# Performance work log

Measured on AMD Instinct MI355X. Metric: run time of the kernel, lower is better.

Reference implementation:

```python
import jax, jax.numpy as jnp
import numpy as np

N_NODES = 50000
N_EDGES = 800000
D_MODEL = 128
N_HEADS = 4
N_LAYERS = 2
F_HEAD = D_MODEL // N_HEADS


def setup_inputs() -> dict:
    key = jax.random.key(0)
    ks = jax.random.split(key, 6)
    x = jax.random.normal(ks[0], (N_NODES, D_MODEL), dtype=jnp.float32)
    edge_index = jax.random.randint(ks[1], (2, N_EDGES), 0, N_NODES, dtype=jnp.int64)
    scale = 1.0 / np.sqrt(D_MODEL)
    W = jax.random.normal(ks[2], (N_LAYERS, D_MODEL, D_MODEL), dtype=jnp.float32) * scale
    a_src = jax.random.normal(ks[3], (N_LAYERS, N_HEADS, F_HEAD), dtype=jnp.float32) * scale
    a_dst = jax.random.normal(ks[4], (N_LAYERS, N_HEADS, F_HEAD), dtype=jnp.float32) * scale
    b = jnp.zeros((N_LAYERS, D_MODEL), dtype=jnp.float32)
    return {"x": x, "edge_index": edge_index, "W": W, "a_src": a_src, "a_dst": a_dst, "b": b}


def _gat_layer(x, src, dst, W_l, a_src_l, a_dst_l, b_l, apply_act):
    N = x.shape[0]
    H, F = a_src_l.shape
    # projected node features, split into heads: [N, H, F]
    h = (x @ W_l).reshape(N, H, F)
    # per-node attention contributions: [N, H]
    alpha_s = jnp.einsum("nhf,hf->nh", h, a_src_l)
    alpha_d = jnp.einsum("nhf,hf->nh", h, a_dst_l)
    # per-edge raw scores, LeakyReLU(0.2): [E, H]
    e = jax.nn.leaky_relu(alpha_s[src] + alpha_d[dst], negative_slope=0.2)
    # numerically-stable segment softmax over edges grouped by target node
    e_max = jax.ops.segment_max(e, dst, num_segments=N)
    e_exp = jnp.exp(e - e_max[dst])
    denom = jax.ops.segment_sum(e_exp, dst, num_segments=N)
    alpha = e_exp / (denom[dst] + 1e-16)  # [E, H]
    # gather source features, weight, scatter-add to targets
    msg = h[src] * alpha[:, :, None]  # [E, H, F]
    out = jax.ops.segment_sum(msg, dst, num_segments=N).reshape(N, H * F)
    out = out + x + b_l  # skip connection (dims match) + bias
    return jax.nn.elu(out) if apply_act else out


def reference(x, edge_index, W, a_src, a_dst, b):
    src, dst = edge_index[0], edge_index[1]
    L = W.shape[0]
    for l in range(L):
        x = _gat_layer(x, src, dst, W[l], a_src[l], a_dst[l], b[l], apply_act=(l < L - 1))
    return x
```

## Files before the change

### kernel.cpp

```cpp
#include <hip/hip_runtime.h>
#include <math.h>

constexpr int NN = 50000;
constexpr int NE = 800000;
constexpr int D  = 128;
constexpr int NH = 4;
constexpr int NBUK = (NN + 255) / 256;
constexpr int CAP  = 4608;
constexpr int FR_PER_LAYER = 9 * 4 * 64;

typedef __attribute__((ext_vector_type(8))) short short8v;
typedef __attribute__((ext_vector_type(4))) float f32x4;

__device__ inline unsigned short rne_bf16(float f) {
    unsigned bits = __float_as_uint(f);
    return (unsigned short)((bits + 0x7FFFu + ((bits >> 16) & 1u)) >> 16);
}

#define DOT2BF(accv, pa, pb) \
    asm("v_dot2_f32_bf16 %0, %1, %2, %0" : "+v"(accv) : "v"(pa), "v"(pb))

__global__ __launch_bounds__(256) void partition_kernel(
    const int* __restrict__ src, const int* __restrict__ dst,
    int* __restrict__ bwp, unsigned* __restrict__ bukbuf)
{
    __shared__ int cnt[NBUK];
    __shared__ int run[NBUK];
    for (int i = threadIdx.x; i < NBUK; i += 256) cnt[i] = 0;
    __syncthreads();
    const int base = blockIdx.x * 2048;
    int s_[8], b_[8], dl_[8];
    #pragma unroll
    for (int i = 0; i < 8; ++i) {
        int e = base + i * 256 + threadIdx.x;
        bool ok = (e < NE);
        s_[i] = ok ? src[e] : 0;
        int d = ok ? dst[e] : 0;
        b_[i] = d >> 8; dl_[i] = d & 255;
        if (ok) atomicAdd(&cnt[b_[i]], 1);
    }
    __syncthreads();
    for (int i = threadIdx.x; i < NBUK; i += 256)
        run[i] = cnt[i] ? atomicAdd(&bwp[i], cnt[i]) : 0;
    __syncthreads();
    #pragma unroll
    for (int i = 0; i < 8; ++i) {
        int e = base + i * 256 + threadIdx.x;
        if (e < NE) {
            int pos = atomicAdd(&run[b_[i]], 1);
            if (pos < CAP)
                bukbuf[b_[i] * CAP + pos] = (unsigned)s_[i] | ((unsigned)dl_[i] << 16);
        }
    }
}

__global__ __launch_bounds__(256) void bucket_sort_kernel(
    const unsigned* __restrict__ bukbuf, const int* __restrict__ bwp,
    int2* __restrict__ rowse, unsigned short* __restrict__ srcs)
{
    const int b = blockIdx.x;
    const int t = threadIdx.x;
    const int cnt = min(bwp[b], CAP);
    const int base = b * CAP;
    __shared__ int hist[256];
    __shared__ int run[256];
    __shared__ int s[256];
    __shared__ unsigned short stage[CAP];
    hist[t] = 0;
    __syncthreads();
    for (int i = t; i < cnt; i += 256)
        atomicAdd(&hist[bukbuf[base + i] >> 16], 1);
    __syncthreads();
    int v = hist[t];
    s[t] = v;
    __syncthreads();
    for (int off = 1; off < 256; off <<= 1) {
        int u = (t >= off) ? s[t - off] : 0;
        __syncthreads();
        s[t] += u;
        __syncthreads();
    }
    const int excl = s[t] - v;
    const int node = b * 256 + t;
    if (node < NN) {
        int2 se; se.x = base + excl; se.y = base + excl + v;
        rowse[node] = se;
    }
    run[t] = excl;
    __syncthreads();
    for (int i = t; i < cnt; i += 256) {
        unsigned p = bukbuf[base + i];
        int pos = atomicAdd(&run[p >> 16], 1);
        stage[pos] = (unsigned short)(p & 0xFFFFu);
    }
    __syncthreads();
    for (int i = t; i < cnt; i += 256) srcs[base + i] = stage[i];
}

__global__ __launch_bounds__(256) void repack_kernel(
    const float* __restrict__ W, const float* __restrict__ a_src,
    const float* __restrict__ a_dst, unsigned short* __restrict__ Wpk,
    int* __restrict__ bwp)
{
    if (blockIdx.x == 0 && threadIdx.x < NBUK) bwp[threadIdx.x] = 0;
    int tid = blockIdx.x * 256 + threadIdx.x;
    if (tid >= 2 * FR_PER_LAYER) return;
    int layer = tid / FR_PER_LAYER;
    int rest  = tid % FR_PER_LAYER;
    int tile  = rest >> 8;
    int kstep = (rest >> 6) & 3;
    int lane  = rest & 63;
    int col   = lane & 15;
    int kbase = kstep * 32 + (lane >> 4) * 8;
    const float* Wl = W + (size_t)layer * D * D;
    unsigned short v[8];
    if (tile < 8) {
        int c = tile * 16 + col;
        #pragma unroll
        for (int j = 0; j < 8; ++j) v[j] = rne_bf16(Wl[(kbase + j) * D + c]);
    } else {
        #pragma unroll
        for (int j = 0; j < 8; ++j) v[j] = 0;
        if (col < 8) {
            const float* av = ((col < 4) ? a_src : a_dst) + layer * D + (col & 3) * 32;
            const int hbase = (col & 3) * 32;
            for (int j = 0; j < 8; ++j) {
                float sum = 0.f;
                const float* wr = Wl + (size_t)(kbase + j) * D + hbase;
                #pragma unroll
                for (int jj = 0; jj < 32; ++jj) sum = fmaf(wr[jj], av[jj], sum);
                v[j] = rne_bf16(sum);
            }
        }
    }
    *(uint4*)(Wpk + (size_t)tid * 8) = *(const uint4*)v;
}

template<int BF16IN>
__global__ __launch_bounds__(256) void gemm_alpha_kernel(
    const void* __restrict__ xin, const unsigned short* __restrict__ Wpk,
    unsigned short* __restrict__ hb, float* __restrict__ alpha_s,
    float* __restrict__ alpha_d)
{
    __shared__ unsigned short xl[64 * 128];
    const int t = threadIdx.x;
    const int row0 = blockIdx.x * 64;

    if constexpr (BF16IN) {
        const unsigned short* xb = (const unsigned short*)xin;
        #pragma unroll
        for (int it = 0; it < 4; ++it) {
            int idx = it * 256 + t;
            int r   = idx >> 4;
            int c8  = (idx & 15) * 8;
            int n   = row0 + r;
            uint4 v = {0u, 0u, 0u, 0u};
            if (n < NN) v = *(const uint4*)(xb + (size_t)n * D + c8);
            *(uint4*)(xl + r * 128 + (c8 ^ ((r & 7) << 3))) = v;
        }
    } else {
        const float* xf = (const float*)xin;
        #pragma unroll
        for (int it = 0; it < 8; ++it) {
            int idx = it * 256 + t;
            int r   = idx >> 5;
            int c4  = (idx & 31) * 4;
            int n   = row0 + r;
            float4 v;
            if (n < NN) v = *(const float4*)(xf + (size_t)n * D + c4);
            else { v.x = 0.f; v.y = 0.f; v.z = 0.f; v.w = 0.f; }
            unsigned p0 = ((unsigned)rne_bf16(v.y) << 16) | rne_bf16(v.x);
            unsigned p1 = ((unsigned)rne_bf16(v.w) << 16) | rne_bf16(v.z);
            uint2 pv; pv.x = p0; pv.y = p1;
            *(uint2*)(xl + r * 128 + (c4 ^ ((r & 7) << 3))) = pv;
        }
    }
    __syncthreads();

    const int wv  = t >> 6;
    const int l   = t & 63;
    const int l15 = l & 15;
    const int g   = l >> 4;
    const int strip = wv * 16;
    const int arow  = strip + l15;

    f32x4 acc[9];
    #pragma unroll
    for (int i = 0; i < 9; ++i) acc[i] = (f32x4){0.f, 0.f, 0.f, 0.f};

    #pragma unroll
    for (int ks = 0; ks < 4; ++ks) {
        const int k0 = ks * 32 + g * 8;
        short8v a = *(const short8v*)(xl + arow * 128 + (k0 ^ ((arow & 7) << 3)));
        #pragma unroll
        for (int tl = 0; tl < 9; ++tl) {
            short8v b = *(const short8v*)(Wpk + ((size_t)(tl * 4 + ks) * 64 + l) * 8);
            acc[tl] = __builtin_amdgcn_mfma_f32_16x16x32_bf16(a, b, acc[tl], 0, 0, 0);
        }
    }

    #pragma unroll
    for (int r = 0; r < 4; ++r) {
        const int n = row0 + strip + g * 4 + r;
        if (n < NN) {
            #pragma unroll
            for (int tl = 0; tl < 8; ++tl)
                hb[(size_t)n * D + tl * 16 + l15] = rne_bf16(acc[tl][r]);
            const float av = acc[8][r];
            if (l15 < 4)      alpha_s[n * NH + l15]       = av;
            else if (l15 < 8) alpha_d[n * NH + (l15 - 4)] = av;
        }
    }
}

#define SHUF2(MI, SA, SB, WP) {                                          \
    int eA = lb + (MI), eB = eA + 1;                                     \
    SA = __shfl(msrc, eA); SB = __shfl(msrc, eB);                        \
    unsigned a01 = (unsigned)__shfl((int)uw01, eA);                      \
    unsigned a23 = (unsigned)__shfl((int)uw23, eA);                      \
    unsigned c01 = (unsigned)__shfl((int)uw01, eB);                      \
    unsigned c23 = (unsigned)__shfl((int)uw23, eB);                      \
    unsigned uwA = (head < 2) ? a01 : a23;                               \
    unsigned uwB = (head < 2) ? c01 : c23;                               \
    WP = __builtin_amdgcn_perm(uwB, uwA, wsel); }

#define ROWLD(S) (*(const uint4*)(hb + ((size_t)(S) << 7) + (ql << 3)))

#define DOT2BLOCK(WP, HA, HB) {                                               \
    DOT2BF(den, WP, ones);                                                    \
    unsigned p_;                                                              \
    p_ = __builtin_amdgcn_perm(HB.x, HA.x, 0x05040100u); DOT2BF(acc[0], p_, WP); \
    p_ = __builtin_amdgcn_perm(HB.x, HA.x, 0x07060302u); DOT2BF(acc[1], p_, WP); \
    p_ = __builtin_amdgcn_perm(HB.y, HA.y, 0x05040100u); DOT2BF(acc[2], p_, WP); \
    p_ = __builtin_amdgcn_perm(HB.y, HA.y, 0x07060302u); DOT2BF(acc[3], p_, WP); \
    p_ = __builtin_amdgcn_perm(HB.z, HA.z, 0x05040100u); DOT2BF(acc[4], p_, WP); \
    p_ = __builtin_amdgcn_perm(HB.z, HA.z, 0x07060302u); DOT2BF(acc[5], p_, WP); \
    p_ = __builtin_amdgcn_perm(HB.w, HA.w, 0x05040100u); DOT2BF(acc[6], p_, WP); \
    p_ = __builtin_amdgcn_perm(HB.w, HA.w, 0x07060302u); DOT2BF(acc[7], p_, WP); }

template<int IN_BF16, int OUT_BF16, int ACT>
__global__ __launch_bounds__(256) void gather_kernel(
    const unsigned short* __restrict__ hb, const float* __restrict__ alpha_s,
    const float* __restrict__ alpha_d, const int2* __restrict__ rowse,
    const unsigned short* __restrict__ srcs, const void* __restrict__ x_in,
    const float* __restrict__ bias, void* __restrict__ out)
{
    const int lane = threadIdx.x & 63;
    const int q    = lane >> 4;
    const int ql   = lane & 15;
    const int head = ql >> 2;
    const int lb   = q * 16;
    const int n = blockIdx.x * 16 + (threadIdx.x >> 6) * 4 + q;
    if (n >= NN) return;

    const int2 se = rowse[n];
    const int start = se.x, end = se.y;
    const float4 ad4 = *(const float4*)&alpha_d[n * NH];
    const unsigned wsel = (head & 1) ? 0x07060302u : 0x05040100u;
    const unsigned ones = 0x3F803F80u;

    float acc[8];
    #pragma unroll
    for (int c = 0; c < 8; ++c) acc[c] = 0.f;
    float den = 0.f;

    for (int base = start; base < end; base += 16) {
        const int cnt = min(16, end - base);
        int msrc = 0;
        unsigned uw01 = 0, uw23 = 0;
        if (ql < cnt) {
            msrc = srcs[base + ql];
            const float4 as4 = *(const float4*)&alpha_s[msrc * NH];
            float e0 = as4.x + ad4.x; e0 = (e0 > 0.f) ? e0 : 0.2f * e0;
            float e1 = as4.y + ad4.y; e1 = (e1 > 0.f) ? e1 : 0.2f * e1;
            float e2 = as4.z + ad4.z; e2 = (e2 > 0.f) ? e2 : 0.2f * e2;
            float e3 = as4.w + ad4.w; e3 = (e3 > 0.f) ? e3 : 0.2f * e3;
            float w0 = __expf(e0), w1 = __expf(e1);
            float w2 = __expf(e2), w3 = __expf(e3);
            uw01 = ((unsigned)rne_bf16(w1) << 16) | rne_bf16(w0);
            uw23 = ((unsigned)rne_bf16(w3) << 16) | rne_bf16(w2);
        }
        const int mm = (cnt + 1) & ~1;

        int sxa, sxb, sya, syb;
        unsigned wpX, wpY;
        uint4 hxa, hxb, hya, hyb;
        SHUF2(0, sxa, sxb, wpX);
        hxa = ROWLD(sxa); hxb = ROWLD(sxb);
        if (mm > 2) {
            SHUF2(2, sya, syb, wpY);
            hya = ROWLD(sya); hyb = ROWLD(syb);
        }
        int m = 0;
        while (true) {
            DOT2BLOCK(wpX, hxa, hxb);
            m += 2;
            if (m >= mm) break;
            if (m + 2 < mm) {
                SHUF2(m + 2, sxa, sxb, wpX);
                hxa = ROWLD(sxa); hxb = ROWLD(sxb);
            }
            DOT2BLOCK(wpY, hya, hyb);
            m += 2;
            if (m >= mm) break;
            if (m + 2 < mm) {
                SHUF2(m + 2, sya, syb, wpY);
                hya = ROWLD(sya); hyb = ROWLD(syb);
            }
        }
    }

    const float inv = 1.f / (den + 1e-16f);
    const size_t o8 = (size_t)n * D + ql * 8;
    float xi[8];
    if constexpr (IN_BF16) {
        const uint4 xv = *(const uint4*)((const unsigned short*)x_in + o8);
        xi[0] = __uint_as_float(xv.x << 16);
        xi[1] = __uint_as_float(xv.x & 0xFFFF0000u);
        xi[2] = __uint_as_float(xv.y << 16);
        xi[3] = __uint_as_float(xv.y & 0xFFFF0000u);
        xi[4] = __uint_as_float(xv.z << 16);
        xi[5] = __uint_as_float(xv.z & 0xFFFF0000u);
        xi[6] = __uint_as_float(xv.w << 16);
        xi[7] = __uint_as_float(xv.w & 0xFFFF0000u);
    } else {
        const float4 a = *(const float4*)((const float*)x_in + o8);
        const float4 b = *(const float4*)((const float*)x_in + o8 + 4);
        xi[0]=a.x; xi[1]=a.y; xi[2]=a.z; xi[3]=a.w;
        xi[4]=b.x; xi[5]=b.y; xi[6]=b.z; xi[7]=b.w;
    }
    const float4 ba = *(const float4*)(bias + ql * 8);
    const float4 bb = *(const float4*)(bias + ql * 8 + 4);
    const float bi[8] = {ba.x, ba.y, ba.z, ba.w, bb.x, bb.y, bb.z, bb.w};
    float o[8];
    #pragma unroll
    for (int c = 0; c < 8; ++c) {
        float v = fmaf(acc[c], inv, xi[c]) + bi[c];
        if constexpr (ACT) v = (v > 0.f) ? v : (__expf(v) - 1.f);
        o[c] = v;
    }
    if constexpr (OUT_BF16) {
        unsigned short ov[8];
        #pragma unroll
        for (int c = 0; c < 8; ++c) ov[c] = rne_bf16(o[c]);
        *(uint4*)((unsigned short*)out + o8) = *(const uint4*)ov;
    } else {
        float4 oa = {o[0], o[1], o[2], o[3]};
        float4 ob = {o[4], o[5], o[6], o[7]};
        *(float4*)((float*)out + o8)     = oa;
        *(float4*)((float*)out + o8 + 4) = ob;
    }
}

extern "C" void kernel_launch(void* const* d_in, const int* in_sizes, int n_in,
                              void* d_out, int out_size, void* d_ws, size_t ws_size,
                              hipStream_t stream) {
    const float* x     = (const float*)d_in[0];
    const int*   ei    = (const int*)d_in[1];
    const float* W     = (const float*)d_in[2];
    const float* a_src = (const float*)d_in[3];
    const float* a_dst = (const float*)d_in[4];
    const float* bias  = (const float*)d_in[5];
    float* outp = (float*)d_out;

    const int* e_src = ei;
    const int* e_dst = ei + NE;

    char* base = (char*)d_ws;
    unsigned short* hb  = (unsigned short*)(base);
    unsigned short* x1b = (unsigned short*)(base + 12800000);
    float* al_s      = (float*)(base + 25600000);
    float* al_d      = (float*)(base + 26400000);
    int2*  rowse     = (int2*) (base + 27200000);
    unsigned short* srcs = (unsigned short*)(base + 27600000);
    unsigned* bukbuf = (unsigned*)(base + 29406336);
    int*   bwp       = (int*)  (base + 33019008);
    unsigned short* Wpk = (unsigned short*)(base + 33019792);

    const int rblocks = (2 * FR_PER_LAYER + 255) / 256;
    repack_kernel<<<rblocks, 256, 0, stream>>>(W, a_src, a_dst, Wpk, bwp);
    const int pblocks = (NE + 2047) / 2048;
    partition_kernel<<<pblocks, 256, 0, stream>>>(e_src, e_dst, bwp, bukbuf);
    bucket_sort_kernel<<<NBUK, 256, 0, stream>>>(bukbuf, bwp, rowse, srcs);

    const int gemm_blocks   = (NN + 63) / 64;
    const int gather_blocks = (NN + 15) / 16;

    gemm_alpha_kernel<0><<<gemm_blocks, 256, 0, stream>>>(x, Wpk, hb, al_s, al_d);
    gather_kernel<0, 1, 1><<<gather_blocks, 256, 0, stream>>>(
        hb, al_s, al_d, rowse, srcs, x, bias, x1b);
    gemm_alpha_kernel<1><<<gemm_blocks, 256, 0, stream>>>(
        x1b, Wpk + (size_t)FR_PER_LAYER * 8, hb, al_s, al_d);
    gather_kernel<1, 0, 0><<<gather_blocks, 256, 0, stream>>>(
        hb, al_s, al_d, rowse, srcs, x1b, bias + D, outp);
}
```

Before: 134.0 us.

## Fuse edge partition with weight repack and bucket sort with first GEMM

```diff
diff --git a/kernel.cpp b/kernel.cpp
--- a/kernel.cpp
+++ b/kernel.cpp
@@ -6,8 +6,11 @@
 constexpr int D  = 128;
 constexpr int NH = 4;
 constexpr int NBUK = (NN + 255) / 256;
-constexpr int CAP  = 4608;
+constexpr int EPB  = 2048;
+constexpr int NPB  = (NE + EPB - 1) / EPB;
+constexpr int CAPS = 4608;
 constexpr int FR_PER_LAYER = 9 * 4 * 64;
+constexpr int RBLK = (2 * FR_PER_LAYER) / 256;
 
 typedef __attribute__((ext_vector_type(8))) short short8v;
 typedef __attribute__((ext_vector_type(4))) float f32x4;
@@ -20,91 +23,10 @@
 #define DOT2BF(accv, pa, pb) \
     asm("v_dot2_f32_bf16 %0, %1, %2, %0" : "+v"(accv) : "v"(pa), "v"(pb))
 
-__global__ __launch_bounds__(256) void partition_kernel(
-    const int* __restrict__ src, const int* __restrict__ dst,
-    int* __restrict__ bwp, unsigned* __restrict__ bukbuf)
-{
-    __shared__ int cnt[NBUK];
-    __shared__ int run[NBUK];
-    for (int i = threadIdx.x; i < NBUK; i += 256) cnt[i] = 0;
-    __syncthreads();
-    const int base = blockIdx.x * 2048;
-    int s_[8], b_[8], dl_[8];
-    #pragma unroll
-    for (int i = 0; i < 8; ++i) {
-        int e = base + i * 256 + threadIdx.x;
-        bool ok = (e < NE);
-        s_[i] = ok ? src[e] : 0;
-        int d = ok ? dst[e] : 0;
-        b_[i] = d >> 8; dl_[i] = d & 255;
-        if (ok) atomicAdd(&cnt[b_[i]], 1);
-    }
-    __syncthreads();
-    for (int i = threadIdx.x; i < NBUK; i += 256)
-        run[i] = cnt[i] ? atomicAdd(&bwp[i], cnt[i]) : 0;
-    __syncthreads();
-    #pragma unroll
-    for (int i = 0; i < 8; ++i) {
-        int e = base + i * 256 + threadIdx.x;
-        if (e < NE) {
-            int pos = atomicAdd(&run[b_[i]], 1);
-            if (pos < CAP)
-                bukbuf[b_[i] * CAP + pos] = (unsigned)s_[i] | ((unsigned)dl_[i] << 16);
-        }
-    }
-}
-
-__global__ __launch_bounds__(256) void bucket_sort_kernel(
-    const unsigned* __restrict__ bukbuf, const int* __restrict__ bwp,
-    int2* __restrict__ rowse, unsigned short* __restrict__ srcs)
-{
-    const int b = blockIdx.x;
-    const int t = threadIdx.x;
-    const int cnt = min(bwp[b], CAP);
-    const int base = b * CAP;
-    __shared__ int hist[256];
-    __shared__ int run[256];
-    __shared__ int s[256];
-    __shared__ unsigned short stage[CAP];
-    hist[t] = 0;
-    __syncthreads();
-    for (int i = t; i < cnt; i += 256)
-        atomicAdd(&hist[bukbuf[base + i] >> 16], 1);
-    __syncthreads();
-    int v = hist[t];
-    s[t] = v;
-    __syncthreads();
-    for (int off = 1; off < 256; off <<= 1) {
-        int u = (t >= off) ? s[t - off] : 0;
-        __syncthreads();
-        s[t] += u;
-        __syncthreads();
-    }
-    const int excl = s[t] - v;
-    const int node = b * 256 + t;
-    if (node < NN) {
-        int2 se; se.x = base + excl; se.y = base + excl + v;
-        rowse[node] = se;
-    }
-    run[t] = excl;
-    __syncthreads();
-    for (int i = t; i < cnt; i += 256) {
-        unsigned p = bukbuf[base + i];
-        int pos = atomicAdd(&run[p >> 16], 1);
-        stage[pos] = (unsigned short)(p & 0xFFFFu);
-    }
-    __syncthreads();
-    for (int i = t; i < cnt; i += 256) srcs[base + i] = stage[i];
-}
-
-__global__ __launch_bounds__(256) void repack_kernel(
-    const float* __restrict__ W, const float* __restrict__ a_src,
-    const float* __restrict__ a_dst, unsigned short* __restrict__ Wpk,
-    int* __restrict__ bwp)
-{
-    if (blockIdx.x == 0 && threadIdx.x < NBUK) bwp[threadIdx.x] = 0;
-    int tid = blockIdx.x * 256 + threadIdx.x;
-    if (tid >= 2 * FR_PER_LAYER) return;
+__device__ __forceinline__ void repack_body(
+    int tid, const float* __restrict__ W, const float* __restrict__ a_src,
+    const float* __restrict__ a_dst, unsigned short* __restrict__ Wpk)
+{
     int layer = tid / FR_PER_LAYER;
     int rest  = tid % FR_PER_LAYER;
     int tile  = rest >> 8;
@@ -136,15 +58,75 @@
     *(uint4*)(Wpk + (size_t)tid * 8) = *(const uint4*)v;
 }
 
+__global__ __launch_bounds__(256) void prep_kernel(
+    const float* __restrict__ W, const float* __restrict__ a_src,
+    const float* __restrict__ a_dst, unsigned short* __restrict__ Wpk,
+    const int* __restrict__ src, const int* __restrict__ dst,
+    unsigned* __restrict__ outbuf, int* __restrict__ cnts,
+    int* __restrict__ lofs)
+{
+    __shared__ union {
+        struct { unsigned stage[EPB]; int cnt[NBUK]; int fill[NBUK]; int sc[256]; } p;
+        int dummy;
+    } sm;
+    if (blockIdx.x < RBLK) {
+        repack_body(blockIdx.x * 256 + threadIdx.x, W, a_src, a_dst, Wpk);
+        return;
+    }
+    const int pb = blockIdx.x - RBLK;
+    const int t  = threadIdx.x;
+    for (int i = t; i < NBUK; i += 256) sm.p.cnt[i] = 0;
+    __syncthreads();
+    const int base = pb * EPB;
+    const int tot  = min(NE - base, EPB);
+    unsigned pk[8]; int bk[8];
+    #pragma unroll
+    for (int i = 0; i < 8; ++i) {
+        int e = base + i * 256 + t;
+        bool ok = (e < NE);
+        int s = ok ? src[e] : 0;
+        int d = ok ? dst[e] : 0;
+        bk[i] = d >> 8;
+        pk[i] = (unsigned)s | ((unsigned)(d & 255) << 16) | ((unsigned)bk[i] << 24);
+        if (ok) atomicAdd(&sm.p.cnt[bk[i]], 1);
+    }
+    __syncthreads();
+    int v = (t < NBUK) ? sm.p.cnt[t] : 0;
+    sm.p.sc[t] = v;
+    __syncthreads();
+    for (int off = 1; off < 256; off <<= 1) {
+        int u = (t >= off) ? sm.p.sc[t - off] : 0;
+        __syncthreads();
+        sm.p.sc[t] += u;
+        __syncthreads();
+    }
+    const int excl = sm.p.sc[t] - v;
+    if (t < NBUK) {
+        sm.p.fill[t] = excl;
+        cnts[t * NPB + pb] = v;
+        lofs[t * NPB + pb] = excl;
+    }
+    __syncthreads();
+    #pragma unroll
+    for (int i = 0; i < 8; ++i) {
+        int e = base + i * 256 + t;
+        if (e < NE) {
+            int pos = atomicAdd(&sm.p.fill[bk[i]], 1);
+            sm.p.stage[pos] = pk[i];
+        }
+    }
+    __syncthreads();
+    for (int i = t; i < tot; i += 256) outbuf[base + i] = sm.p.stage[i];
+}
+
 template<int BF16IN>
-__global__ __launch_bounds__(256) void gemm_alpha_kernel(
-    const void* __restrict__ xin, const unsigned short* __restrict__ Wpk,
-    unsigned short* __restrict__ hb, float* __restrict__ alpha_s,
-    float* __restrict__ alpha_d)
-{
-    __shared__ unsigned short xl[64 * 128];
+__device__ __forceinline__ void gemm_body(
+    int blk, unsigned short* __restrict__ xl, const void* __restrict__ xin,
+    const unsigned short* __restrict__ Wpk, unsigned short* __restrict__ hb,
+    float* __restrict__ alpha_s, float* __restrict__ alpha_d)
+{
     const int t = threadIdx.x;
-    const int row0 = blockIdx.x * 64;
+    const int row0 = blk * 64;
 
     if constexpr (BF16IN) {
         const unsigned short* xb = (const unsigned short*)xin;
@@ -211,6 +193,77 @@
             else if (l15 < 8) alpha_d[n * NH + (l15 - 4)] = av;
         }
     }
+}
+
+template<int BF16IN>
+__global__ __launch_bounds__(256) void sort_gemm_kernel(
+    const unsigned* __restrict__ outbuf, const int* __restrict__ cnts,
+    const int* __restrict__ lofs, int2* __restrict__ rowse,
+    unsigned short* __restrict__ srcs, const void* __restrict__ xin,
+    const unsigned short* __restrict__ Wpk, unsigned short* __restrict__ hb,
+    float* __restrict__ alpha_s, float* __restrict__ alpha_d)
+{
+    __shared__ union {
+        struct { unsigned stage[CAPS]; int hist[256]; int run[256]; int sc[256]; int cursor; } s;
+        unsigned short xl[64 * 128];
+    } sm;
+
+    if (blockIdx.x >= NBUK) {
+        gemm_body<BF16IN>(blockIdx.x - NBUK, sm.xl, xin, Wpk, hb, alpha_s, alpha_d);
+        return;
+    }
+    const int b = blockIdx.x;
+    const int t = threadIdx.x;
+    if (t == 0) sm.s.cursor = 0;
+    sm.s.hist[t] = 0;
+    __syncthreads();
+    for (int pb = t; pb < NPB; pb += 256) {
+        int len = cnts[b * NPB + pb];
+        if (len > 0) {
+            int off = lofs[b * NPB + pb];
+            int pos = atomicAdd(&sm.s.cursor, len);
+            const unsigned* sp = outbuf + pb * EPB + off;
+            for (int k = 0; k < len; ++k)
+                if (pos + k < CAPS) sm.s.stage[pos + k] = sp[k];
+        }
+    }
+    __syncthreads();
+    const int tot = min(sm.s.cursor, CAPS);
+    for (int i = t; i < tot; i += 256)
+        atomicAdd(&sm.s.hist[(sm.s.stage[i] >> 16) & 255], 1);
+    __syncthreads();
+    int v = sm.s.hist[t];
+    sm.s.sc[t] = v;
+    __syncthreads();
+    for (int off = 1; off < 256; off <<= 1) {
+        int u = (t >= off) ? sm.s.sc[t - off] : 0;
+        __syncthreads();
+        sm.s.sc[t] += u;
+        __syncthreads();
+    }
+    const int excl = sm.s.sc[t] - v;
+    const int node = b * 256 + t;
+    if (node < NN) {
+        int2 se; se.x = b * CAPS + excl; se.y = b * CAPS + excl + v;
+        rowse[node] = se;
+    }
+    sm.s.run[t] = excl;
+    __syncthreads();
+    for (int i = t; i < tot; i += 256) {
+        unsigned p = sm.s.stage[i];
+        int pos = atomicAdd(&sm.s.run[(p >> 16) & 255], 1);
+        srcs[b * CAPS + pos] = (unsigned short)(p & 0xFFFFu);
+    }
+}
+
+template<int BF16IN>
+__global__ __launch_bounds__(256) void gemm_alpha_kernel(
+    const void* __restrict__ xin, const unsigned short* __restrict__ Wpk,
+    unsigned short* __restrict__ hb, float* __restrict__ alpha_s,
+    float* __restrict__ alpha_d)
+{
+    __shared__ unsigned short xl[64 * 128];
+    gemm_body<BF16IN>(blockIdx.x, xl, xin, Wpk, hb, alpha_s, alpha_d);
 }
 
 #define SHUF2(MI, SA, SB, WP) {                                          \
@@ -373,24 +426,26 @@
     float* al_d      = (float*)(base + 26400000);
     int2*  rowse     = (int2*) (base + 27200000);
     unsigned short* srcs = (unsigned short*)(base + 27600000);
-    unsigned* bukbuf = (unsigned*)(base + 29406336);
-    int*   bwp       = (int*)  (base + 33019008);
-    unsigned short* Wpk = (unsigned short*)(base + 33019792);
-
-    const int rblocks = (2 * FR_PER_LAYER + 255) / 256;
-    repack_kernel<<<rblocks, 256, 0, stream>>>(W, a_src, a_dst, Wpk, bwp);
-    const int pblocks = (NE + 2047) / 2048;
-    partition_kernel<<<pblocks, 256, 0, stream>>>(e_src, e_dst, bwp, bukbuf);
-    bucket_sort_kernel<<<NBUK, 256, 0, stream>>>(bukbuf, bwp, rowse, srcs);
+    unsigned* outbuf = (unsigned*)(base + 29406336);
+    int* cnts        = (int*)  (base + 32609408);
+    int* lofs        = (int*)  (base + 32915952);
+    unsigned short* Wpk = (unsigned short*)(base + 33222496);
+
+    prep_kernel<<<RBLK + NPB, 256, 0, stream>>>(W, a_src, a_dst, Wpk,
+                                                e_src, e_dst, outbuf, cnts, lofs);
 
     const int gemm_blocks   = (NN + 63) / 64;
     const int gather_blocks = (NN + 15) / 16;
 
-    gemm_alpha_kernel<0><<<gemm_blocks, 256, 0, stream>>>(x, Wpk, hb, al_s, al_d);
+    sort_gemm_kernel<0><<<NBUK + gemm_blocks, 256, 0, stream>>>(
+        outbuf, cnts, lofs, rowse, srcs, x, Wpk, hb, al_s, al_d);
+
     gather_kernel<0, 1, 1><<<gather_blocks, 256, 0, stream>>>(
         hb, al_s, al_d, rowse, srcs, x, bias, x1b);
+
     gemm_alpha_kernel<1><<<gemm_blocks, 256, 0, stream>>>(
         x1b, Wpk + (size_t)FR_PER_LAYER * 8, hb, al_s, al_d);
+
     gather_kernel<1, 0, 0><<<gather_blocks, 256, 0, stream>>>(
         hb, al_s, al_d, rowse, srcs, x1b, bias + D, outp);
 }
```

New measurement: 125.0 us (median of 2 runs). 6.7% less time.
